# Kernel optimization log

Hardware: AMD Instinct MI355X
Metric: run time of the kernel (lower is better)

The kernel has to match this reference:

```python
import jax, jax.numpy as jnp
import numpy as np

TAU = 2.0        # spikingjelly LIFNode default
V_TH = 1.0       # default v_threshold
V_RESET = 0.0    # default v_reset (hard reset)


def setup_inputs() -> dict:
    key = jax.random.key(0)
    k1, k2, k3 = jax.random.split(key, 3)
    T, B, N, Cin, Cout = 4, 8, 1024, 512, 512
    x = jax.random.normal(k1, (T, B, N, Cin), dtype=jnp.float32)
    # nn.Linear weights are [out, in]; kaiming-uniform-ish scale
    W1 = jax.random.normal(k2, (Cout, Cin), dtype=jnp.float32) / np.sqrt(Cin)
    W2 = jax.random.normal(k3, (Cout, Cout), dtype=jnp.float32) / np.sqrt(Cout)
    return {"x": x, "W1": W1, "W2": W2}


def _spike(v):
    # forward heaviside (ATan surrogate only matters for backward)
    return (v >= V_TH).astype(v.dtype)


def _lif_multistep(h):
    # h: [T, B, N, C]; multi-step LIF with decay_input=True, hard reset to 0
    v0 = jnp.zeros(h.shape[1:], dtype=h.dtype)

    def step(v, x_t):
        v = v + (x_t - (v - V_RESET)) / TAU   # leaky integration
        s = _spike(v)                          # threshold
        v = v * (1.0 - s) + V_RESET * s        # hard reset
        return v, s

    _, spikes = jax.lax.scan(step, v0, h)
    return spikes  # [T, B, N, C]


def reference(x, W1, W2):
    h = jnp.einsum('tbni,oi->tbno', x, W1)      # Linear(in_ch, out_ch, bias=False)
    s = _lif_multistep(h)                        # LIFNode, step_mode='m'
    out = jnp.einsum('tbno,po->tbnp', s, W2)    # Linear(out_ch, out_ch, bias=False)
    return out.astype(jnp.float32)
```

## Files before the change

### kernel.cpp

```cpp
#include <hip/hip_runtime.h>


typedef _Float16 half8  __attribute__((ext_vector_type(8)));
typedef _Float16 half4v __attribute__((ext_vector_type(4)));
typedef float    f32x4  __attribute__((ext_vector_type(4)));

constexpr int TT   = 4;
constexpr int BB   = 8;
constexpr int NN   = 1024;
constexpr int CC   = 512;
constexpr int MROW = BB * NN;
constexpr int MTOT = TT * MROW;
constexpr int BNC  = MROW * CC;
constexpr int LDK  = 40;
constexpr int LTS  = 68;

__global__ __launch_bounds__(256)
void gemm1_chain(const float* __restrict__ X, const float* __restrict__ W,
                 float* __restrict__ H) {
#pragma clang fp contract(off)
    __shared__ float At[16][LTS];
    __shared__ float Bt[16][LTS];

    const int tid  = threadIdx.x;
    const int RM   = blockIdx.x * 64;
    const int CN   = blockIdx.y * 64;
    const int tx   = tid & 15;
    const int ty   = tid >> 4;
    const int srow = tid >> 2;
    const int sc4  = (tid & 3) * 4;

    float acc[4][4] = {};

    for (int k0 = 0; k0 < CC; k0 += 16) {
        __syncthreads();
        f32x4 va = *(const f32x4*)&X[(size_t)(RM + srow) * CC + k0 + sc4];
        f32x4 vb = *(const f32x4*)&W[(size_t)(CN + srow) * CC + k0 + sc4];
#pragma unroll
        for (int e = 0; e < 4; ++e) {
            At[sc4 + e][srow] = va[e];
            Bt[sc4 + e][srow] = vb[e];
        }
        __syncthreads();
#pragma unroll
        for (int k = 0; k < 16; ++k) {
            f32x4 a = *(const f32x4*)&At[k][ty * 4];
            f32x4 b = *(const f32x4*)&Bt[k][tx * 4];
#pragma unroll
            for (int i = 0; i < 4; ++i)
#pragma unroll
                for (int j = 0; j < 4; ++j)
                    acc[i][j] = __builtin_fmaf(a[i], b[j], acc[i][j]);
        }
    }

#pragma unroll
    for (int i = 0; i < 4; ++i)
#pragma unroll
        for (int j = 0; j < 4; ++j)
            H[(size_t)(RM + ty * 4 + i) * CC + CN + tx * 4 + j] = acc[i][j];
}

__global__ __launch_bounds__(256)
void lif_np(const float* __restrict__ H, _Float16* __restrict__ S) {
#pragma clang fp contract(off)
    int g = blockIdx.x * 256 + threadIdx.x;
    float v[4] = {0.f, 0.f, 0.f, 0.f};
#pragma unroll
    for (int t = 0; t < TT; ++t) {
        f32x4 h = *(const f32x4*)&H[(size_t)t * BNC + (size_t)g * 4];
        half4v s;
#pragma unroll
        for (int e = 0; e < 4; ++e) {
            float d  = h[e] - v[e];
            float d2 = d * 0.5f;
            v[e] = v[e] + d2;
            bool sp = v[e] >= 1.0f;
            s[e] = sp ? (_Float16)1.0f : (_Float16)0.0f;
            if (sp) v[e] = 0.0f;
        }
        *(half4v*)&S[(size_t)t * BNC + (size_t)g * 4] = s;
    }
}

__global__ __launch_bounds__(256)
void gemm2_f16(const _Float16* __restrict__ S, const float* __restrict__ W,
               float* __restrict__ O) {
    __shared__ _Float16 As[128][LDK], Bs[128][LDK];

    const int tid  = threadIdx.x;
    const int RM   = blockIdx.x * 128;
    const int CN   = blockIdx.y * 128;
    const int lane = tid & 63;
    const int wv   = tid >> 6;
    const int wr   = (wv >> 1) * 64;
    const int wc   = (wv & 1) * 64;
    const int r15  = lane & 15;
    const int kg   = lane >> 4;

    f32x4 acc[4][4] = {};

    for (int k0 = 0; k0 < CC; k0 += 32) {
        __syncthreads();
#pragma unroll
        for (int j = 0; j < 2; ++j) {
            int id  = tid + 256 * j;
            int row = id >> 2;
            int c8  = (id & 3) * 8;
            *(half8*)&As[row][c8] =
                *(const half8*)&S[(size_t)(RM + row) * CC + k0 + c8];
        }
#pragma unroll
        for (int j = 0; j < 4; ++j) {
            int id  = tid + 256 * j;
            int row = id >> 3;
            int c4  = (id & 7) * 4;
            f32x4 v = *(const f32x4*)&W[(size_t)(CN + row) * CC + k0 + c4];
            half4v hv;
#pragma unroll
            for (int e = 0; e < 4; ++e) hv[e] = (_Float16)v[e];
            *(half4v*)&Bs[row][c4] = hv;
        }
        __syncthreads();

        half8 a[4], b[4];
#pragma unroll
        for (int i = 0; i < 4; ++i) {
            a[i] = *(const half8*)&As[wr + i * 16 + r15][kg * 8];
            b[i] = *(const half8*)&Bs[wc + i * 16 + r15][kg * 8];
        }
#pragma unroll
        for (int i = 0; i < 4; ++i)
#pragma unroll
            for (int j = 0; j < 4; ++j)
                acc[i][j] = __builtin_amdgcn_mfma_f32_16x16x32_f16(a[i], b[j], acc[i][j], 0, 0, 0);
    }

#pragma unroll
    for (int i = 0; i < 4; ++i)
#pragma unroll
        for (int j = 0; j < 4; ++j)
#pragma unroll
            for (int r = 0; r < 4; ++r) {
                int gm = RM + wr + i * 16 + kg * 4 + r;
                int gn = CN + wc + j * 16 + r15;
                O[(size_t)gm * CC + gn] = acc[i][j][r];
            }
}

extern "C" void kernel_launch(void* const* d_in, const int* in_sizes, int n_in,
                              void* d_out, int out_size, void* d_ws, size_t ws_size,
                              hipStream_t stream) {
    const float* x  = (const float*)d_in[0];
    const float* W1 = (const float*)d_in[1];
    const float* W2 = (const float*)d_in[2];
    float* out = (float*)d_out;

    float*    h = out;
    _Float16* s = (_Float16*)d_ws;

    dim3 g1(MTOT / 64, CC / 64);
    gemm1_chain<<<g1, 256, 0, stream>>>(x, W1, h);

    lif_np<<<BNC / 4 / 256, 256, 0, stream>>>(h, s);

    dim3 g2(MTOT / 128, CC / 128);
    gemm2_f16<<<g2, 256, 0, stream>>>(s, W2, out);
}
```

Baseline: 293.7 us.

## Retile fp32 GEMM1 with register-blocked B from transposed weights and pack spikes as bytes

Adds a small kernel that transposes W1 into workspace. GEMM1 is rewritten so each thread computes a 4x16 output tile: the X tile lives in double-buffered LDS, and the weight row for each k is read as a wave-uniform 64-byte vector straight from global memory. This raises FMA work per LDS read and overlaps the next X tile load with compute. Spikes are now stored as one byte each (the high byte of fp16 1.0) and expanded to fp16 while GEMM2 loads its tile, halving spike traffic. The cost is an extra launch, and the transposed weights share workspace with the spike buffer, which relies on kernel ordering.

```diff
diff --git a/kernel.cpp b/kernel.cpp
--- a/kernel.cpp
+++ b/kernel.cpp
@@ -4,6 +4,8 @@
 typedef _Float16 half8  __attribute__((ext_vector_type(8)));
 typedef _Float16 half4v __attribute__((ext_vector_type(4)));
 typedef float    f32x4  __attribute__((ext_vector_type(4)));
+typedef float    f32x16 __attribute__((ext_vector_type(16)));
+typedef unsigned short ushort8 __attribute__((ext_vector_type(8)));
 
 constexpr int TT   = 4;
 constexpr int BB   = 8;
@@ -13,78 +15,121 @@
 constexpr int MTOT = TT * MROW;
 constexpr int BNC  = MROW * CC;
 constexpr int LDK  = 40;
-constexpr int LTS  = 68;
+constexpr int LTA  = 260;
 
 __global__ __launch_bounds__(256)
-void gemm1_chain(const float* __restrict__ X, const float* __restrict__ W,
-                 float* __restrict__ H) {
+void transpose_w(const float* __restrict__ W, float* __restrict__ Wt) {
+    __shared__ float T[64][65];
+    const int tid = threadIdx.x;
+    const int bo  = blockIdx.x * 64;
+    const int bk  = blockIdx.y * 64;
+#pragma unroll
+    for (int j = 0; j < 16; ++j) {
+        int id = tid + 256 * j;
+        int r = id >> 6, c = id & 63;
+        T[r][c] = W[(size_t)(bo + r) * CC + bk + c];
+    }
+    __syncthreads();
+#pragma unroll
+    for (int j = 0; j < 16; ++j) {
+        int id = tid + 256 * j;
+        int r = id >> 6, c = id & 63;
+        Wt[(size_t)(bk + r) * CC + bo + c] = T[c][r];
+    }
+}
+
+__global__ __launch_bounds__(512, 4)
+void gemm1_smem(const float* __restrict__ X, const float* __restrict__ Wt,
+                float* __restrict__ H) {
 #pragma clang fp contract(off)
-    __shared__ float At[16][LTS];
-    __shared__ float Bt[16][LTS];
+    __shared__ float At[2][32][LTA];
 
     const int tid  = threadIdx.x;
-    const int RM   = blockIdx.x * 64;
-    const int CN   = blockIdx.y * 64;
-    const int tx   = tid & 15;
-    const int ty   = tid >> 4;
-    const int srow = tid >> 2;
-    const int sc4  = (tid & 3) * 4;
-
-    float acc[4][4] = {};
-
-    for (int k0 = 0; k0 < CC; k0 += 16) {
-        __syncthreads();
-        f32x4 va = *(const f32x4*)&X[(size_t)(RM + srow) * CC + k0 + sc4];
-        f32x4 vb = *(const f32x4*)&W[(size_t)(CN + srow) * CC + k0 + sc4];
-#pragma unroll
-        for (int e = 0; e < 4; ++e) {
-            At[sc4 + e][srow] = va[e];
-            Bt[sc4 + e][srow] = vb[e];
-        }
-        __syncthreads();
-#pragma unroll
-        for (int k = 0; k < 16; ++k) {
-            f32x4 a = *(const f32x4*)&At[k][ty * 4];
-            f32x4 b = *(const f32x4*)&Bt[k][tx * 4];
+    const int lane = tid & 63;
+    const int wid  = __builtin_amdgcn_readfirstlane(tid >> 6);
+    const int RM   = blockIdx.x * 256;
+    const int CN   = blockIdx.y * 128 + wid * 16;
+    const float* wcol = Wt + CN;
+
+    const int srow = tid >> 1;
+    const int sk16 = (tid & 1) * 16;
+
+    float acc[4][16] = {};
+    f32x4 rx[4];
+
+#pragma unroll
+    for (int q = 0; q < 4; ++q)
+        rx[q] = *(const f32x4*)&X[(size_t)(RM + srow) * CC + sk16 + q * 4];
+#pragma unroll
+    for (int q = 0; q < 4; ++q)
+#pragma unroll
+        for (int e = 0; e < 4; ++e)
+            At[0][sk16 + q * 4 + e][srow] = rx[q][e];
+    __syncthreads();
+
+    for (int kt = 0; kt < 16; ++kt) {
+        const int cur = kt & 1;
+        if (kt < 15) {
+            int kk = (kt + 1) * 32;
+#pragma unroll
+            for (int q = 0; q < 4; ++q)
+                rx[q] = *(const f32x4*)&X[(size_t)(RM + srow) * CC + kk + sk16 + q * 4];
+        }
+#pragma unroll 4
+        for (int k = 0; k < 32; ++k) {
+            f32x4 a = *(const f32x4*)&At[cur][k][lane * 4];
+            f32x16 b = *(const f32x16*)&wcol[(size_t)(kt * 32 + k) * CC];
 #pragma unroll
             for (int i = 0; i < 4; ++i)
 #pragma unroll
-                for (int j = 0; j < 4; ++j)
+                for (int j = 0; j < 16; ++j)
                     acc[i][j] = __builtin_fmaf(a[i], b[j], acc[i][j]);
         }
-    }
-
-#pragma unroll
-    for (int i = 0; i < 4; ++i)
-#pragma unroll
-        for (int j = 0; j < 4; ++j)
-            H[(size_t)(RM + ty * 4 + i) * CC + CN + tx * 4 + j] = acc[i][j];
+        if (kt < 15) {
+#pragma unroll
+            for (int q = 0; q < 4; ++q)
+#pragma unroll
+                for (int e = 0; e < 4; ++e)
+                    At[cur ^ 1][sk16 + q * 4 + e][srow] = rx[q][e];
+            __syncthreads();
+        }
+    }
+
+#pragma unroll
+    for (int i = 0; i < 4; ++i) {
+        size_t base = (size_t)(RM + lane * 4 + i) * CC + CN;
+#pragma unroll
+        for (int q = 0; q < 4; ++q) {
+            f32x4 o = {acc[i][q * 4], acc[i][q * 4 + 1],
+                       acc[i][q * 4 + 2], acc[i][q * 4 + 3]};
+            *(f32x4*)&H[base + q * 4] = o;
+        }
+    }
 }
 
 __global__ __launch_bounds__(256)
-void lif_np(const float* __restrict__ H, _Float16* __restrict__ S) {
+void lif_np(const float* __restrict__ H, unsigned char* __restrict__ S8) {
 #pragma clang fp contract(off)
     int g = blockIdx.x * 256 + threadIdx.x;
     float v[4] = {0.f, 0.f, 0.f, 0.f};
 #pragma unroll
     for (int t = 0; t < TT; ++t) {
         f32x4 h = *(const f32x4*)&H[(size_t)t * BNC + (size_t)g * 4];
-        half4v s;
+        unsigned int pack = 0;
 #pragma unroll
         for (int e = 0; e < 4; ++e) {
             float d  = h[e] - v[e];
             float d2 = d * 0.5f;
             v[e] = v[e] + d2;
             bool sp = v[e] >= 1.0f;
-            s[e] = sp ? (_Float16)1.0f : (_Float16)0.0f;
-            if (sp) v[e] = 0.0f;
-        }
-        *(half4v*)&S[(size_t)t * BNC + (size_t)g * 4] = s;
+            if (sp) { pack |= 0x3Cu << (8 * e); v[e] = 0.0f; }
+        }
+        *(unsigned int*)&S8[(size_t)t * BNC + (size_t)g * 4] = pack;
     }
 }
 
 __global__ __launch_bounds__(256)
-void gemm2_f16(const _Float16* __restrict__ S, const float* __restrict__ W,
+void gemm2_f16(const unsigned char* __restrict__ S8, const float* __restrict__ W,
                float* __restrict__ O) {
     __shared__ _Float16 As[128][LDK], Bs[128][LDK];
 
@@ -107,8 +152,13 @@
             int id  = tid + 256 * j;
             int row = id >> 2;
             int c8  = (id & 3) * 8;
-            *(half8*)&As[row][c8] =
-                *(const half8*)&S[(size_t)(RM + row) * CC + k0 + c8];
+            unsigned long long v =
+                *(const unsigned long long*)&S8[(size_t)(RM + row) * CC + k0 + c8];
+            ushort8 u;
+#pragma unroll
+            for (int e = 0; e < 8; ++e)
+                u[e] = (unsigned short)(((v >> (8 * e)) & 0xFFull) << 8);
+            *(ushort8*)&As[row][c8] = u;
         }
 #pragma unroll
         for (int j = 0; j < 4; ++j) {
@@ -156,14 +206,18 @@
     const float* W2 = (const float*)d_in[2];
     float* out = (float*)d_out;
 
-    float*    h = out;
-    _Float16* s = (_Float16*)d_ws;
-
-    dim3 g1(MTOT / 64, CC / 64);
-    gemm1_chain<<<g1, 256, 0, stream>>>(x, W1, h);
-
-    lif_np<<<BNC / 4 / 256, 256, 0, stream>>>(h, s);
+    float*         h  = out;
+    unsigned char* s8 = (unsigned char*)d_ws;
+    float*         wt = (float*)((char*)d_ws + (size_t)BNC);
+
+    dim3 gt(CC / 64, CC / 64);
+    transpose_w<<<gt, 256, 0, stream>>>(W1, wt);
+
+    dim3 g1(MTOT / 256, CC / 128);
+    gemm1_smem<<<g1, 512, 0, stream>>>(x, wt, h);
+
+    lif_np<<<BNC / 4 / 256, 256, 0, stream>>>(h, s8);
 
     dim3 g2(MTOT / 128, CC / 128);
-    gemm2_f16<<<g2, 256, 0, stream>>>(s, W2, out);
-}
+    gemm2_f16<<<g2, 256, 0, stream>>>(s8, W2, out);
+}
```

Result: faster. 239.7 us (-18.4%).
